# Kernel optimization log

Measured on AMD Instinct MI355X. Metric: run time of the kernel, lower is better.

## Reference

```python
import jax, jax.numpy as jnp
import numpy as np

NEG_INF = -1e30  # large negative instead of float('-inf') for fp16/bf16 safety in softmax


def setup_inputs() -> dict:
    key = jax.random.key(0)
    k1, k2, k3, k4 = jax.random.split(key, 4)
    B, T, C, H = 8, 2048, 768, 64
    x = jax.random.normal(k1, (B, T, C), dtype=jnp.float32)
    # nn.Linear(n_embd, head_size, bias=False): y = x @ W.T, W shape (head_size, n_embd)
    s = 1.0 / np.sqrt(C)
    Wk = jax.random.uniform(k2, (H, C), dtype=jnp.float32, minval=-s, maxval=s)
    Wq = jax.random.uniform(k3, (H, C), dtype=jnp.float32, minval=-s, maxval=s)
    Wv = jax.random.uniform(k4, (H, C), dtype=jnp.float32, minval=-s, maxval=s)
    return {"x": x, "Wk": Wk, "Wq": Wq, "Wv": Wv}


def reference(x, Wk, Wq, Wv):
    # x: [B,T,C]; Wk/Wq/Wv: [H,C]
    k = jnp.einsum('btc,hc->bth', x, Wk)  # [B,T,H]
    q = jnp.einsum('btc,hc->bth', x, Wq)
    v = jnp.einsum('btc,hc->bth', x, Wv)
    att = jnp.einsum('bqh,bkh->bqk', q, k)  # [B,T,T], NOTE: no 1/sqrt(H) scaling, faithful to source
    T = x.shape[1]
    causal = jnp.tril(jnp.ones((T, T), dtype=bool))
    att = jnp.where(causal, att, NEG_INF)
    att = jax.nn.softmax(att, axis=-1)
    out = jnp.einsum('bqk,bkh->bqh', att, v)  # [B,T,H]
    return out
```

## Files before the change

kernel.cpp:

```cpp
#include <hip/hip_runtime.h>
#include <hip/hip_bf16.h>
#include <stdint.h>

typedef float    f32x4  __attribute__((ext_vector_type(4)));
typedef float    f32x16 __attribute__((ext_vector_type(16)));
typedef short    s16x8  __attribute__((ext_vector_type(8)));
typedef uint32_t u32x4  __attribute__((ext_vector_type(4)));

#define NB 8
#define NT 2048
#define NC 768
#define NH 64

__device__ __forceinline__ uint32_t f2bf1(float f) {
  union { float f; uint32_t u; } v; v.f = f;
  uint32_t u = v.u;
  return (u + 0x7fffu + ((u >> 16) & 1u)) >> 16;
}
__device__ __forceinline__ uint32_t packbf2(float lo, float hi) {
  return f2bf1(lo) | (f2bf1(hi) << 16);
}

__global__ __launch_bounds__(256) void wconv_kernel(
    const float* __restrict__ Wk, const float* __restrict__ Wq,
    const float* __restrict__ Wv, short* __restrict__ Wb)
{
  int idx = blockIdx.x * 256 + threadIdx.x;
  if (idx >= 192 * 768) return;
  int n = idx / 768;
  float v;
  if (n < 64)       v = Wq[idx];
  else if (n < 128) v = Wk[idx - 64 * 768];
  else              v = Wv[idx - 128 * 768];
  Wb[idx] = (short)f2bf1(v);
}

__global__ __launch_bounds__(256) void proj_kernel(
    const float* __restrict__ x, const short* __restrict__ Wb,
    short* __restrict__ qb, short* __restrict__ kb, short* __restrict__ vTb)
{
  __shared__ char smem[8192 + 24576];
  short* ldsX   = (short*)smem;
  float* ldsAcc = (float*)(smem + 8192);
  short* ldsV   = (short*)smem;

  const int tid  = threadIdx.x;
  const int lane = tid & 63;
  const int w    = tid >> 6;
  const int kh   = w >> 1;
  const int nh   = w & 1;
  const int col  = lane & 31;
  const int half = lane >> 5;
  const int t0   = blockIdx.x * 32;

  f32x16 acc[3];
#pragma unroll
  for (int j = 0; j < 3; ++j)
#pragma unroll
    for (int e = 0; e < 16; ++e) acc[j][e] = 0.f;

  const int sg  = tid & 127;
  const int skh = tid >> 7;
  const int sr  = sg >> 2;
  const int sf  = (sg & 3) * 16;
  const float* xsrc = x + (size_t)(t0 + sr) * NC + skh * 384 + sf;
  short* ldst = ldsX + skh * 2048 + sr * 64 + sf;

  f32x4 st[4];
#pragma unroll
  for (int u = 0; u < 4; ++u) st[u] = *(const f32x4*)(xsrc + u * 4);

  const short* wbase = Wb + kh * 384 + half * 8;

  for (int s = 0; s < 6; ++s) {
    __syncthreads();
    {
      uint32_t pw[8];
#pragma unroll
      for (int u = 0; u < 4; ++u) {
        pw[2 * u]     = packbf2(st[u][0], st[u][1]);
        pw[2 * u + 1] = packbf2(st[u][2], st[u][3]);
      }
      *(u32x4*)ldst       = (u32x4){pw[0], pw[1], pw[2], pw[3]};
      *(u32x4*)(ldst + 8) = (u32x4){pw[4], pw[5], pw[6], pw[7]};
    }
    __syncthreads();
    if (s < 5) {
#pragma unroll
      for (int u = 0; u < 4; ++u) st[u] = *(const f32x4*)(xsrc + (s + 1) * 64 + u * 4);
    }
#pragma unroll
    for (int ks = 0; ks < 4; ++ks) {
      s16x8 af = *(const s16x8*)&ldsX[kh * 2048 + col * 64 + ks * 16 + half * 8];
#pragma unroll
      for (int j = 0; j < 3; ++j) {
        int n = (nh * 3 + j) * 32 + col;
        s16x8 bf = *(const s16x8*)(wbase + (size_t)n * NC + s * 64 + ks * 16);
        acc[j] = __builtin_amdgcn_mfma_f32_32x32x16_bf16(af, bf, acc[j], 0, 0, 0);
      }
    }
  }

  if (kh == 0) {
#pragma unroll
    for (int j = 0; j < 3; ++j)
#pragma unroll
      for (int r = 0; r < 16; ++r) {
        int rd = (r & 3) + 8 * (r >> 2) + 4 * half;
        ldsAcc[rd * 192 + (nh * 3 + j) * 32 + col] = acc[j][r];
      }
  }
  __syncthreads();
  const int b  = t0 >> 11;
  const int tl = t0 & (NT - 1);
  if (kh == 1) {
#pragma unroll
    for (int j = 0; j < 3; ++j) {
      int nb = (nh * 3 + j) * 32;
#pragma unroll
      for (int r = 0; r < 16; ++r) {
        int rd = (r & 3) + 8 * (r >> 2) + 4 * half;
        float sum = acc[j][r] + ldsAcc[rd * 192 + nb + col];
        if (nb < 128) {
          short* dst = (nb < 64) ? qb : kb;
          dst[(size_t)(t0 + rd) * NH + (nb & 63) + col] = (short)f2bf1(sum);
        } else {
          ldsV[(nb - 128 + col) * 32 + rd] = (short)f2bf1(sum);
        }
      }
    }
  }
  __syncthreads();
  {
    int h = tid >> 2, off = (tid & 3) * 8;
    *(s16x8*)&vTb[(size_t)(b * NH + h) * NT + tl + off] = *(const s16x8*)&ldsV[h * 32 + off];
  }
}

__global__ __launch_bounds__(256) void attn_kernel(
    const short* __restrict__ qb, const short* __restrict__ kb,
    const short* __restrict__ vTb, float* __restrict__ out)
{
  __shared__ float ldsO[4][32][65];
  __shared__ float ldsM[4][32];
  __shared__ float ldsL[4][32];

  const int tid  = threadIdx.x;
  const int lane = tid & 63;
  const int w    = tid >> 6;
  const int col  = lane & 31;
  const int half = lane >> 5;
  const int b    = blockIdx.x >> 6;
  int qt = blockIdx.x & 63;
  if (blockIdx.x & 256) qt = 63 - qt;
  const int q0 = qt * 32;
  const int nT = qt + 1;
  const int tBeg = (w * nT) >> 2;
  const int tEnd = ((w + 1) * nT) >> 2;

  s16x8 qf[4];
  {
    const short* qptr = qb + (size_t)(b * NT + q0 + col) * NH + half * 8;
#pragma unroll
    for (int ks = 0; ks < 4; ++ks) qf[ks] = *(const s16x8*)(qptr + ks * 16);
  }

  const short* kbase = kb  + (size_t)(b * NT + col) * NH + half * 8;
  const short* vbase = vTb + (size_t)(b * NH + col) * NT + half * 8;

  f32x16 oacc[2];
#pragma unroll
  for (int t = 0; t < 2; ++t)
#pragma unroll
    for (int e = 0; e < 16; ++e) oacc[t][e] = 0.f;

  float m = -1e30f, l = 0.f;

  s16x8 rk[4], rv[4];
  auto prefetch = [&](int t) {
#pragma unroll
    for (int ks = 0; ks < 4; ++ks)
      rk[ks] = *(const s16x8*)(kbase + (size_t)t * 32 * NH + ks * 16);
#pragma unroll
    for (int i = 0; i < 4; ++i)
      rv[i] = *(const s16x8*)(vbase + (size_t)(i >> 1) * 32 * NT + t * 32 + (i & 1) * 16);
  };
  if (tBeg < tEnd) prefetch(tBeg);

  for (int t = tBeg; t < tEnd; ++t) {
    s16x8 ck[4] = {rk[0], rk[1], rk[2], rk[3]};
    s16x8 cv[4] = {rv[0], rv[1], rv[2], rv[3]};
    if (t + 1 < tEnd) prefetch(t + 1);

    f32x16 s;
#pragma unroll
    for (int e = 0; e < 16; ++e) s[e] = 0.f;
#pragma unroll
    for (int ks = 0; ks < 4; ++ks)
      s = __builtin_amdgcn_mfma_f32_32x32x16_bf16(ck[ks], qf[ks], s, 0, 0, 0);

    if (t == nT - 1) {
#pragma unroll
      for (int r = 0; r < 16; ++r) {
        int rd = (r & 3) + 8 * (r >> 2) + 4 * half;
        if (rd > col) s[r] = -1e30f;
      }
    }
    float vmax = s[0];
#pragma unroll
    for (int r = 1; r < 16; ++r) vmax = fmaxf(vmax, s[r]);
    vmax = fmaxf(vmax, __shfl_xor(vmax, 32));
    float mn    = fmaxf(m, vmax);
    float alpha = __expf(m - mn);
    float p[16];
    float rs = 0.f;
#pragma unroll
    for (int r = 0; r < 16; ++r) { p[r] = __expf(s[r] - mn); rs += p[r]; }
    rs += __shfl_xor(rs, 32);
    l = l * alpha + rs;
    m = mn;
#pragma unroll
    for (int t2 = 0; t2 < 2; ++t2)
#pragma unroll
      for (int e = 0; e < 16; ++e) oacc[t2][e] *= alpha;

    uint32_t pw[8];
#pragma unroll
    for (int i = 0; i < 8; ++i) pw[i] = packbf2(p[2 * i], p[2 * i + 1]);
#pragma unroll
    for (int kc = 0; kc < 2; ++kc) {
      uint32_t s0 = half ? pw[4 * kc]     : pw[4 * kc + 2];
      uint32_t s1 = half ? pw[4 * kc + 1] : pw[4 * kc + 3];
      uint32_t r0 = __shfl_xor(s0, 32);
      uint32_t r1 = __shfl_xor(s1, 32);
      uint32_t w0 = half ? r0 : pw[4 * kc];
      uint32_t w1 = half ? r1 : pw[4 * kc + 1];
      uint32_t w2 = half ? pw[4 * kc + 2] : r0;
      uint32_t w3 = half ? pw[4 * kc + 3] : r1;
      union { u32x4 u; s16x8 v; } pf;
      pf.u = (u32x4){w0, w1, w2, w3};
#pragma unroll
      for (int ht = 0; ht < 2; ++ht)
        oacc[ht] = __builtin_amdgcn_mfma_f32_32x32x16_bf16(cv[ht * 2 + kc], pf.v, oacc[ht], 0, 0, 0);
    }
  }

  if (half == 0) { ldsM[w][col] = m; ldsL[w][col] = l; }
#pragma unroll
  for (int ht = 0; ht < 2; ++ht)
#pragma unroll
    for (int r = 0; r < 16; ++r) {
      int rd = (r & 3) + 8 * (r >> 2) + 4 * half;
      ldsO[w][col][ht * 32 + rd] = oacc[ht][r];
    }
  __syncthreads();

  const int q  = tid >> 3;
  const int h0 = (tid & 7) * 8;
  float mv[4], lv[4];
#pragma unroll
  for (int i = 0; i < 4; ++i) { mv[i] = ldsM[i][q]; lv[i] = ldsL[i][q]; }
  float M = fmaxf(fmaxf(mv[0], mv[1]), fmaxf(mv[2], mv[3]));
  float cf[4], L = 0.f;
#pragma unroll
  for (int i = 0; i < 4; ++i) { cf[i] = __expf(mv[i] - M); L += cf[i] * lv[i]; }
  float inv = 1.0f / L;
  float o[8];
#pragma unroll
  for (int j = 0; j < 8; ++j) {
    float a = 0.f;
#pragma unroll
    for (int i = 0; i < 4; ++i) a += cf[i] * ldsO[i][q][h0 + j];
    o[j] = a * inv;
  }
  float* obase = out + (size_t)(b * NT + q0 + q) * NH + h0;
  *(f32x4*)obase       = (f32x4){o[0], o[1], o[2], o[3]};
  *(f32x4*)(obase + 4) = (f32x4){o[4], o[5], o[6], o[7]};
}

extern "C" void kernel_launch(void* const* d_in, const int* in_sizes, int n_in,
                              void* d_out, int out_size, void* d_ws, size_t ws_size,
                              hipStream_t stream) {
  const float* x  = (const float*)d_in[0];
  const float* Wk = (const float*)d_in[1];
  const float* Wq = (const float*)d_in[2];
  const float* Wv = (const float*)d_in[3];
  float* out = (float*)d_out;

  char* ws = (char*)d_ws;
  short* Wb  = (short*)(ws);
  short* qb  = (short*)(ws + 524288);
  short* kb  = (short*)(ws + 524288 + 2097152);
  short* vTb = (short*)(ws + 524288 + 2 * 2097152);

  hipLaunchKernelGGL(wconv_kernel, dim3(576), dim3(256), 0, stream, Wk, Wq, Wv, Wb);
  hipLaunchKernelGGL(proj_kernel,  dim3(512), dim3(256), 0, stream, x, Wb, qb, kb, vTb);
  hipLaunchKernelGGL(attn_kernel,  dim3(512), dim3(256), 0, stream, qb, kb, vTb, out);
}
```

Baseline: 132.7 us.

## Use 8 waves per attention block with tree merge, exp2 softmax, bulk-staged projection

The attention kernel now runs 512 threads (8 waves), each handling an eighth of the key tiles. Partial softmax states are combined with a log-tree merge in LDS, and the output is staged through LDS for coalesced stores. Q is pre-scaled by log2(e) so the softmax can use exp2f. The projection kernel loads the whole 32x768 x tile into swizzled LDS in one shot instead of a 6-stage loop, and packs pairs with the HIP bf16x2 intrinsic. These aim at more latency hiding and less exp and sync cost, at the price of more LDS and register pressure and extra barriers during the merge.

```diff
diff --git a/kernel.cpp b/kernel.cpp
--- a/kernel.cpp
+++ b/kernel.cpp
@@ -11,6 +11,7 @@
 #define NT 2048
 #define NC 768
 #define NH 64
+#define LOG2E 1.4426950408889634f
 
 __device__ __forceinline__ uint32_t f2bf1(float f) {
   union { float f; uint32_t u; } v; v.f = f;
@@ -18,7 +19,9 @@
   return (u + 0x7fffu + ((u >> 16) & 1u)) >> 16;
 }
 __device__ __forceinline__ uint32_t packbf2(float lo, float hi) {
-  return f2bf1(lo) | (f2bf1(hi) << 16);
+  union { __hip_bfloat162 h; uint32_t u; } c;
+  c.h = __float22bfloat162_rn(float2{lo, hi});
+  return c.u;
 }
 
 __global__ __launch_bounds__(256) void wconv_kernel(
@@ -35,14 +38,14 @@
   Wb[idx] = (short)f2bf1(v);
 }
 
-__global__ __launch_bounds__(256) void proj_kernel(
+__global__ __launch_bounds__(256, 2) void proj_kernel(
     const float* __restrict__ x, const short* __restrict__ Wb,
     short* __restrict__ qb, short* __restrict__ kb, short* __restrict__ vTb)
 {
-  __shared__ char smem[8192 + 24576];
+  __shared__ char smem[49152 + 4096];
   short* ldsX   = (short*)smem;
-  float* ldsAcc = (float*)(smem + 8192);
-  short* ldsV   = (short*)smem;
+  float* ldsAcc = (float*)smem;
+  short* ldsV   = (short*)(smem + 49152);
 
   const int tid  = threadIdx.x;
   const int lane = tid & 63;
@@ -53,54 +56,48 @@
   const int half = lane >> 5;
   const int t0   = blockIdx.x * 32;
 
+  {
+    const int tok = tid >> 3;
+    const int g   = tid & 7;
+    const float* src = x + (size_t)(t0 + tok) * NC + g * 8;
+    f32x4 st[12][2];
+#pragma unroll
+    for (int c = 0; c < 12; ++c) {
+      st[c][0] = *(const f32x4*)(src + c * 64);
+      st[c][1] = *(const f32x4*)(src + c * 64 + 4);
+    }
+    short* dst = ldsX + tok * 64 + ((g ^ (tok & 7)) << 3);
+#pragma unroll
+    for (int c = 0; c < 12; ++c) {
+      u32x4 pw = {packbf2(st[c][0][0], st[c][0][1]), packbf2(st[c][0][2], st[c][0][3]),
+                  packbf2(st[c][1][0], st[c][1][1]), packbf2(st[c][1][2], st[c][1][3])};
+      *(u32x4*)(dst + c * 2048) = pw;
+    }
+  }
+  __syncthreads();
+
   f32x16 acc[3];
 #pragma unroll
   for (int j = 0; j < 3; ++j)
 #pragma unroll
     for (int e = 0; e < 16; ++e) acc[j][e] = 0.f;
 
-  const int sg  = tid & 127;
-  const int skh = tid >> 7;
-  const int sr  = sg >> 2;
-  const int sf  = (sg & 3) * 16;
-  const float* xsrc = x + (size_t)(t0 + sr) * NC + skh * 384 + sf;
-  short* ldst = ldsX + skh * 2048 + sr * 64 + sf;
-
-  f32x4 st[4];
-#pragma unroll
-  for (int u = 0; u < 4; ++u) st[u] = *(const f32x4*)(xsrc + u * 4);
-
-  const short* wbase = Wb + kh * 384 + half * 8;
-
-  for (int s = 0; s < 6; ++s) {
-    __syncthreads();
-    {
-      uint32_t pw[8];
-#pragma unroll
-      for (int u = 0; u < 4; ++u) {
-        pw[2 * u]     = packbf2(st[u][0], st[u][1]);
-        pw[2 * u + 1] = packbf2(st[u][2], st[u][3]);
-      }
-      *(u32x4*)ldst       = (u32x4){pw[0], pw[1], pw[2], pw[3]};
-      *(u32x4*)(ldst + 8) = (u32x4){pw[4], pw[5], pw[6], pw[7]};
-    }
-    __syncthreads();
-    if (s < 5) {
-#pragma unroll
-      for (int u = 0; u < 4; ++u) st[u] = *(const f32x4*)(xsrc + (s + 1) * 64 + u * 4);
-    }
+#pragma unroll
+  for (int c6 = 0; c6 < 6; ++c6) {
+    const int c = kh * 6 + c6;
 #pragma unroll
     for (int ks = 0; ks < 4; ++ks) {
-      s16x8 af = *(const s16x8*)&ldsX[kh * 2048 + col * 64 + ks * 16 + half * 8];
+      s16x8 af = *(const s16x8*)&ldsX[c * 2048 + col * 64 + (((ks * 2 + half) ^ (col & 7)) << 3)];
 #pragma unroll
       for (int j = 0; j < 3; ++j) {
         int n = (nh * 3 + j) * 32 + col;
-        s16x8 bf = *(const s16x8*)(wbase + (size_t)n * NC + s * 64 + ks * 16);
+        s16x8 bf = *(const s16x8*)&Wb[(size_t)n * NC + c * 64 + ks * 16 + half * 8];
         acc[j] = __builtin_amdgcn_mfma_f32_32x32x16_bf16(af, bf, acc[j], 0, 0, 0);
       }
     }
   }
 
+  __syncthreads();
   if (kh == 0) {
 #pragma unroll
     for (int j = 0; j < 3; ++j)
@@ -121,9 +118,10 @@
       for (int r = 0; r < 16; ++r) {
         int rd = (r & 3) + 8 * (r >> 2) + 4 * half;
         float sum = acc[j][r] + ldsAcc[rd * 192 + nb + col];
-        if (nb < 128) {
-          short* dst = (nb < 64) ? qb : kb;
-          dst[(size_t)(t0 + rd) * NH + (nb & 63) + col] = (short)f2bf1(sum);
+        if (nb < 64) {
+          qb[(size_t)(t0 + rd) * NH + nb + col] = (short)f2bf1(sum * LOG2E);
+        } else if (nb < 128) {
+          kb[(size_t)(t0 + rd) * NH + (nb - 64) + col] = (short)f2bf1(sum);
         } else {
           ldsV[(nb - 128 + col) * 32 + rd] = (short)f2bf1(sum);
         }
@@ -137,7 +135,7 @@
   }
 }
 
-__global__ __launch_bounds__(256) void attn_kernel(
+__global__ __launch_bounds__(512, 4) void attn_kernel(
     const short* __restrict__ qb, const short* __restrict__ kb,
     const short* __restrict__ vTb, float* __restrict__ out)
 {
@@ -155,8 +153,8 @@
   if (blockIdx.x & 256) qt = 63 - qt;
   const int q0 = qt * 32;
   const int nT = qt + 1;
-  const int tBeg = (w * nT) >> 2;
-  const int tEnd = ((w + 1) * nT) >> 2;
+  const int tBeg = (w * nT) >> 3;
+  const int tEnd = ((w + 1) * nT) >> 3;
 
   s16x8 qf[4];
   {
@@ -211,11 +209,11 @@
     for (int r = 1; r < 16; ++r) vmax = fmaxf(vmax, s[r]);
     vmax = fmaxf(vmax, __shfl_xor(vmax, 32));
     float mn    = fmaxf(m, vmax);
-    float alpha = __expf(m - mn);
+    float alpha = exp2f(m - mn);
     float p[16];
     float rs = 0.f;
 #pragma unroll
-    for (int r = 0; r < 16; ++r) { p[r] = __expf(s[r] - mn); rs += p[r]; }
+    for (int r = 0; r < 16; ++r) { p[r] = exp2f(s[r] - mn); rs += p[r]; }
     rs += __shfl_xor(rs, 32);
     l = l * alpha + rs;
     m = mn;
@@ -245,37 +243,58 @@
     }
   }
 
-  if (half == 0) { ldsM[w][col] = m; ldsL[w][col] = l; }
-#pragma unroll
-  for (int ht = 0; ht < 2; ++ht)
-#pragma unroll
-    for (int r = 0; r < 16; ++r) {
-      int rd = (r & 3) + 8 * (r >> 2) + 4 * half;
-      ldsO[w][col][ht * 32 + rd] = oacc[ht][r];
-    }
-  __syncthreads();
-
-  const int q  = tid >> 3;
-  const int h0 = (tid & 7) * 8;
-  float mv[4], lv[4];
-#pragma unroll
-  for (int i = 0; i < 4; ++i) { mv[i] = ldsM[i][q]; lv[i] = ldsL[i][q]; }
-  float M = fmaxf(fmaxf(mv[0], mv[1]), fmaxf(mv[2], mv[3]));
-  float cf[4], L = 0.f;
-#pragma unroll
-  for (int i = 0; i < 4; ++i) { cf[i] = __expf(mv[i] - M); L += cf[i] * lv[i]; }
-  float inv = 1.0f / L;
-  float o[8];
-#pragma unroll
-  for (int j = 0; j < 8; ++j) {
-    float a = 0.f;
-#pragma unroll
-    for (int i = 0; i < 4; ++i) a += cf[i] * ldsO[i][q][h0 + j];
-    o[j] = a * inv;
-  }
-  float* obase = out + (size_t)(b * NT + q0 + q) * NH + h0;
-  *(f32x4*)obase       = (f32x4){o[0], o[1], o[2], o[3]};
-  *(f32x4*)(obase + 4) = (f32x4){o[4], o[5], o[6], o[7]};
+  auto writeSlot = [&](int slot) {
+    if (half == 0) { ldsM[slot][col] = m; ldsL[slot][col] = l; }
+#pragma unroll
+    for (int ht = 0; ht < 2; ++ht)
+#pragma unroll
+      for (int r = 0; r < 16; ++r) {
+        int rd = (r & 3) + 8 * (r >> 2) + 4 * half;
+        ldsO[slot][col][ht * 32 + rd] = oacc[ht][r];
+      }
+  };
+  auto mergeFrom = [&](int slot) {
+    float mb = ldsM[slot][col];
+    float lb = ldsL[slot][col];
+    float M2 = fmaxf(m, mb);
+    float ca = exp2f(m - M2), cb = exp2f(mb - M2);
+    l = ca * l + cb * lb;
+    m = M2;
+#pragma unroll
+    for (int ht = 0; ht < 2; ++ht)
+#pragma unroll
+      for (int r = 0; r < 16; ++r) {
+        int rd = (r & 3) + 8 * (r >> 2) + 4 * half;
+        oacc[ht][r] = ca * oacc[ht][r] + cb * ldsO[slot][col][ht * 32 + rd];
+      }
+  };
+
+  if (w >= 4) writeSlot(w - 4);
+  __syncthreads();
+  if (w < 4) mergeFrom(w);
+  __syncthreads();
+  if (w == 2 || w == 3) writeSlot(w - 2);
+  __syncthreads();
+  if (w < 2) mergeFrom(w);
+  __syncthreads();
+  if (w == 1) writeSlot(0);
+  __syncthreads();
+  if (w == 0) {
+    mergeFrom(0);
+    float inv = 1.0f / l;
+#pragma unroll
+    for (int ht = 0; ht < 2; ++ht)
+#pragma unroll
+      for (int r = 0; r < 16; ++r) {
+        int rd = (r & 3) + 8 * (r >> 2) + 4 * half;
+        ldsO[0][col][ht * 32 + rd] = oacc[ht][r] * inv;
+      }
+  }
+  __syncthreads();
+  {
+    int q = tid >> 4, off = (tid & 15) * 4;
+    *(f32x4*)(out + (size_t)(b * NT + q0 + q) * NH + off) = *(const f32x4*)&ldsO[0][q][off];
+  }
 }
 
 extern "C" void kernel_launch(void* const* d_in, const int* in_sizes, int n_in,
@@ -295,5 +314,5 @@
 
   hipLaunchKernelGGL(wconv_kernel, dim3(576), dim3(256), 0, stream, Wk, Wq, Wv, Wb);
   hipLaunchKernelGGL(proj_kernel,  dim3(512), dim3(256), 0, stream, x, Wb, qb, kb, vTb);
-  hipLaunchKernelGGL(attn_kernel,  dim3(512), dim3(256), 0, stream, qb, kb, vTb, out);
-}
+  hipLaunchKernelGGL(attn_kernel,  dim3(512), dim3(512), 0, stream, qb, kb, vTb, out);
+}
```

Result: slower. 148.6 us (+12.0%).

## Store Q/K/V in MFMA fragment layout, restructure projection and double-buffer attention

Applied to the files above, without the earlier changes.

The projection kernel now runs 512 threads with a 4-way K split. It loads x directly from global memory into registers and converts it to bf16 without staging through LDS, then reduces the partial sums through LDS. Q, K and V are written in a pre-swizzled MFMA-fragment layout, with Q pre-scaled by log2(e), so attention can use exp2 and issue contiguous per-lane loads. The attention loop now double-buffers K/V tiles across two register sets, and bf16 packing uses the HIP intrinsic. Together these aim to cut LDS traffic and load latency, at the cost of higher register pressure and extra sync stages in the reduction.

```diff
diff --git a/kernel.cpp b/kernel.cpp
--- a/kernel.cpp
+++ b/kernel.cpp
@@ -11,6 +11,7 @@
 #define NT 2048
 #define NC 768
 #define NH 64
+#define LOG2E 1.4426950408889634f
 
 __device__ __forceinline__ uint32_t f2bf1(float f) {
   union { float f; uint32_t u; } v; v.f = f;
@@ -18,7 +19,9 @@
   return (u + 0x7fffu + ((u >> 16) & 1u)) >> 16;
 }
 __device__ __forceinline__ uint32_t packbf2(float lo, float hi) {
-  return f2bf1(lo) | (f2bf1(hi) << 16);
+  union { __hip_bfloat162 h; uint32_t u; } c;
+  c.h = __float22bfloat162_rn(float2{lo, hi});
+  return c.u;
 }
 
 __global__ __launch_bounds__(256) void wconv_kernel(
@@ -35,14 +38,14 @@
   Wb[idx] = (short)f2bf1(v);
 }
 
-__global__ __launch_bounds__(256) void proj_kernel(
+__global__ __launch_bounds__(512, 2) void proj_kernel(
     const float* __restrict__ x, const short* __restrict__ Wb,
-    short* __restrict__ qb, short* __restrict__ kb, short* __restrict__ vTb)
+    short* __restrict__ qf_buf, short* __restrict__ kf_buf, short* __restrict__ vf_buf)
 {
-  __shared__ char smem[8192 + 24576];
-  short* ldsX   = (short*)smem;
-  float* ldsAcc = (float*)(smem + 8192);
-  short* ldsV   = (short*)smem;
+  __shared__ float slots[4 * 3072];
+  short* ldsQT = (short*)slots;
+  short* ldsKT = (short*)slots + 2176;
+  short* ldsVT = (short*)slots + 4352;
 
   const int tid  = threadIdx.x;
   const int lane = tid & 63;
@@ -53,93 +56,113 @@
   const int half = lane >> 5;
   const int t0   = blockIdx.x * 32;
 
+  const float* xsrc = x + (size_t)(t0 + col) * NC + kh * 192 + half * 8;
+  const short* w0 = Wb + (size_t)((nh * 3 + 0) * 32 + col) * NC + kh * 192 + half * 8;
+  const short* w1 = w0 + 32 * NC;
+  const short* w2 = w1 + 32 * NC;
+
   f32x16 acc[3];
 #pragma unroll
   for (int j = 0; j < 3; ++j)
 #pragma unroll
     for (int e = 0; e < 16; ++e) acc[j][e] = 0.f;
 
-  const int sg  = tid & 127;
-  const int skh = tid >> 7;
-  const int sr  = sg >> 2;
-  const int sf  = (sg & 3) * 16;
-  const float* xsrc = x + (size_t)(t0 + sr) * NC + skh * 384 + sf;
-  short* ldst = ldsX + skh * 2048 + sr * 64 + sf;
-
-  f32x4 st[4];
-#pragma unroll
-  for (int u = 0; u < 4; ++u) st[u] = *(const f32x4*)(xsrc + u * 4);
-
-  const short* wbase = Wb + kh * 384 + half * 8;
-
-  for (int s = 0; s < 6; ++s) {
-    __syncthreads();
-    {
-      uint32_t pw[8];
-#pragma unroll
-      for (int u = 0; u < 4; ++u) {
-        pw[2 * u]     = packbf2(st[u][0], st[u][1]);
-        pw[2 * u + 1] = packbf2(st[u][2], st[u][3]);
-      }
-      *(u32x4*)ldst       = (u32x4){pw[0], pw[1], pw[2], pw[3]};
-      *(u32x4*)(ldst + 8) = (u32x4){pw[4], pw[5], pw[6], pw[7]};
-    }
-    __syncthreads();
-    if (s < 5) {
-#pragma unroll
-      for (int u = 0; u < 4; ++u) st[u] = *(const f32x4*)(xsrc + (s + 1) * 64 + u * 4);
-    }
-#pragma unroll
-    for (int ks = 0; ks < 4; ++ks) {
-      s16x8 af = *(const s16x8*)&ldsX[kh * 2048 + col * 64 + ks * 16 + half * 8];
-#pragma unroll
-      for (int j = 0; j < 3; ++j) {
-        int n = (nh * 3 + j) * 32 + col;
-        s16x8 bf = *(const s16x8*)(wbase + (size_t)n * NC + s * 64 + ks * 16);
-        acc[j] = __builtin_amdgcn_mfma_f32_32x32x16_bf16(af, bf, acc[j], 0, 0, 0);
-      }
-    }
-  }
-
+  f32x4 xA[2], xB[2];
+  s16x8 wA[3], wB[3];
+  auto loadS = [&](f32x4* xr, s16x8* wr, int ks) {
+    xr[0] = *(const f32x4*)(xsrc + ks * 16);
+    xr[1] = *(const f32x4*)(xsrc + ks * 16 + 4);
+    wr[0] = *(const s16x8*)(w0 + ks * 16);
+    wr[1] = *(const s16x8*)(w1 + ks * 16);
+    wr[2] = *(const s16x8*)(w2 + ks * 16);
+  };
+  auto computeS = [&](f32x4* xr, s16x8* wr) {
+    union { u32x4 u; s16x8 v; } af;
+    af.u = (u32x4){packbf2(xr[0][0], xr[0][1]), packbf2(xr[0][2], xr[0][3]),
+                   packbf2(xr[1][0], xr[1][1]), packbf2(xr[1][2], xr[1][3])};
+    acc[0] = __builtin_amdgcn_mfma_f32_32x32x16_bf16(af.v, wr[0], acc[0], 0, 0, 0);
+    acc[1] = __builtin_amdgcn_mfma_f32_32x32x16_bf16(af.v, wr[1], acc[1], 0, 0, 0);
+    acc[2] = __builtin_amdgcn_mfma_f32_32x32x16_bf16(af.v, wr[2], acc[2], 0, 0, 0);
+  };
+
+  loadS(xA, wA, 0);
+#pragma unroll
+  for (int ks = 0; ks < 12; ks += 2) {
+    loadS(xB, wB, ks + 1);
+    computeS(xA, wA);
+    if (ks + 2 < 12) loadS(xA, wA, ks + 2);
+    computeS(xB, wB);
+  }
+
+  if (kh >= 2) {
+    float* sl = slots + ((kh - 2) * 2 + nh) * 3072;
+#pragma unroll
+    for (int j = 0; j < 3; ++j)
+#pragma unroll
+      for (int r = 0; r < 16; ++r) {
+        int rd = (r & 3) + 8 * (r >> 2) + 4 * half;
+        sl[rd * 96 + j * 32 + col] = acc[j][r];
+      }
+  }
+  __syncthreads();
+  if (kh < 2) {
+    float* sl = slots + (kh * 2 + nh) * 3072;
+#pragma unroll
+    for (int j = 0; j < 3; ++j)
+#pragma unroll
+      for (int r = 0; r < 16; ++r) {
+        int rd = (r & 3) + 8 * (r >> 2) + 4 * half;
+        acc[j][r] += sl[rd * 96 + j * 32 + col];
+      }
+  }
+  __syncthreads();
+  if (kh == 1) {
+    float* sl = slots + (2 + nh) * 3072;
+#pragma unroll
+    for (int j = 0; j < 3; ++j)
+#pragma unroll
+      for (int r = 0; r < 16; ++r) {
+        int rd = (r & 3) + 8 * (r >> 2) + 4 * half;
+        sl[rd * 96 + j * 32 + col] = acc[j][r];
+      }
+  }
+  __syncthreads();
   if (kh == 0) {
+    float* sl = slots + (2 + nh) * 3072;
 #pragma unroll
     for (int j = 0; j < 3; ++j)
 #pragma unroll
       for (int r = 0; r < 16; ++r) {
         int rd = (r & 3) + 8 * (r >> 2) + 4 * half;
-        ldsAcc[rd * 192 + (nh * 3 + j) * 32 + col] = acc[j][r];
-      }
-  }
-  __syncthreads();
-  const int b  = t0 >> 11;
-  const int tl = t0 & (NT - 1);
-  if (kh == 1) {
-#pragma unroll
-    for (int j = 0; j < 3; ++j) {
-      int nb = (nh * 3 + j) * 32;
-#pragma unroll
-      for (int r = 0; r < 16; ++r) {
-        int rd = (r & 3) + 8 * (r >> 2) + 4 * half;
-        float sum = acc[j][r] + ldsAcc[rd * 192 + nb + col];
-        if (nb < 128) {
-          short* dst = (nb < 64) ? qb : kb;
-          dst[(size_t)(t0 + rd) * NH + (nb & 63) + col] = (short)f2bf1(sum);
-        } else {
-          ldsV[(nb - 128 + col) * 32 + rd] = (short)f2bf1(sum);
-        }
-      }
-    }
-  }
-  __syncthreads();
+        float sum = acc[j][r] + sl[rd * 96 + j * 32 + col];
+        int nn = nh * 96 + j * 32 + col;
+        if (nn < 64)        ldsQT[rd * 68 + nn]        = (short)f2bf1(sum * LOG2E);
+        else if (nn < 128)  ldsKT[rd * 68 + (nn - 64)] = (short)f2bf1(sum);
+        else                ldsVT[(nn - 128) * 34 + rd] = (short)f2bf1(sum);
+      }
+  }
+  __syncthreads();
+
   {
-    int h = tid >> 2, off = (tid & 3) * 8;
-    *(s16x8*)&vTb[(size_t)(b * NH + h) * NT + tl + off] = *(const s16x8*)&ldsV[h * 32 + off];
-  }
-}
-
-__global__ __launch_bounds__(256) void attn_kernel(
-    const short* __restrict__ qb, const short* __restrict__ kb,
-    const short* __restrict__ vTb, float* __restrict__ out)
+    const int b  = t0 >> 11;
+    const int kt = (t0 >> 5) & 63;
+    const size_t base = ((size_t)(b * 64 + kt) * 4) * 512;
+    if (w < 4) {
+      s16x8 vq = *(const s16x8*)&ldsQT[col * 68 + w * 16 + half * 8];
+      *(s16x8*)&qf_buf[base + w * 512 + lane * 8] = vq;
+      s16x8 vk = *(const s16x8*)&ldsKT[col * 68 + w * 16 + half * 8];
+      *(s16x8*)&kf_buf[base + w * 512 + lane * 8] = vk;
+    } else {
+      int i = w - 4;
+      s16x8 vv = *(const s16x8*)&ldsVT[(col + (i >> 1) * 32) * 34 + (i & 1) * 16 + half * 8];
+      *(s16x8*)&vf_buf[base + i * 512 + lane * 8] = vv;
+    }
+  }
+}
+
+__global__ __launch_bounds__(256, 2) void attn_kernel(
+    const short* __restrict__ qf_buf, const short* __restrict__ kf_buf,
+    const short* __restrict__ vf_buf, float* __restrict__ out)
 {
   __shared__ float ldsO[4][32][65];
   __shared__ float ldsM[4][32];
@@ -160,38 +183,31 @@
 
   s16x8 qf[4];
   {
-    const short* qptr = qb + (size_t)(b * NT + q0 + col) * NH + half * 8;
-#pragma unroll
-    for (int ks = 0; ks < 4; ++ks) qf[ks] = *(const s16x8*)(qptr + ks * 16);
-  }
-
-  const short* kbase = kb  + (size_t)(b * NT + col) * NH + half * 8;
-  const short* vbase = vTb + (size_t)(b * NH + col) * NT + half * 8;
+    const short* qp = qf_buf + ((size_t)(b * 64 + qt) * 4) * 512 + lane * 8;
+#pragma unroll
+    for (int ks = 0; ks < 4; ++ks) qf[ks] = *(const s16x8*)(qp + ks * 512);
+  }
+  const short* kfb = kf_buf + (size_t)b * 64 * 2048 + lane * 8;
+  const short* vfb = vf_buf + (size_t)b * 64 * 2048 + lane * 8;
 
   f32x16 oacc[2];
 #pragma unroll
-  for (int t = 0; t < 2; ++t)
-#pragma unroll
-    for (int e = 0; e < 16; ++e) oacc[t][e] = 0.f;
-
+  for (int i = 0; i < 2; ++i)
+#pragma unroll
+    for (int e = 0; e < 16; ++e) oacc[i][e] = 0.f;
   float m = -1e30f, l = 0.f;
 
-  s16x8 rk[4], rv[4];
-  auto prefetch = [&](int t) {
-#pragma unroll
-    for (int ks = 0; ks < 4; ++ks)
-      rk[ks] = *(const s16x8*)(kbase + (size_t)t * 32 * NH + ks * 16);
-#pragma unroll
-    for (int i = 0; i < 4; ++i)
-      rv[i] = *(const s16x8*)(vbase + (size_t)(i >> 1) * 32 * NT + t * 32 + (i & 1) * 16);
+  s16x8 kA[4], vA[4], kB[4], vB[4];
+  auto loadT = [&](s16x8* dk, s16x8* dv, int t) {
+    const short* kp = kfb + (size_t)t * 2048;
+    const short* vp = vfb + (size_t)t * 2048;
+#pragma unroll
+    for (int i = 0; i < 4; ++i) {
+      dk[i] = *(const s16x8*)(kp + i * 512);
+      dv[i] = *(const s16x8*)(vp + i * 512);
+    }
   };
-  if (tBeg < tEnd) prefetch(tBeg);
-
-  for (int t = tBeg; t < tEnd; ++t) {
-    s16x8 ck[4] = {rk[0], rk[1], rk[2], rk[3]};
-    s16x8 cv[4] = {rv[0], rv[1], rv[2], rv[3]};
-    if (t + 1 < tEnd) prefetch(t + 1);
-
+  auto body = [&](s16x8* ck, s16x8* cv, int t) {
     f32x16 s;
 #pragma unroll
     for (int e = 0; e < 16; ++e) s[e] = 0.f;
@@ -211,18 +227,18 @@
     for (int r = 1; r < 16; ++r) vmax = fmaxf(vmax, s[r]);
     vmax = fmaxf(vmax, __shfl_xor(vmax, 32));
     float mn    = fmaxf(m, vmax);
-    float alpha = __expf(m - mn);
+    float alpha = exp2f(m - mn);
     float p[16];
     float rs = 0.f;
 #pragma unroll
-    for (int r = 0; r < 16; ++r) { p[r] = __expf(s[r] - mn); rs += p[r]; }
+    for (int r = 0; r < 16; ++r) { p[r] = exp2f(s[r] - mn); rs += p[r]; }
     rs += __shfl_xor(rs, 32);
     l = l * alpha + rs;
     m = mn;
 #pragma unroll
-    for (int t2 = 0; t2 < 2; ++t2)
-#pragma unroll
-      for (int e = 0; e < 16; ++e) oacc[t2][e] *= alpha;
+    for (int i = 0; i < 2; ++i)
+#pragma unroll
+      for (int e = 0; e < 16; ++e) oacc[i][e] *= alpha;
 
     uint32_t pw[8];
 #pragma unroll
@@ -243,7 +259,18 @@
       for (int ht = 0; ht < 2; ++ht)
         oacc[ht] = __builtin_amdgcn_mfma_f32_32x32x16_bf16(cv[ht * 2 + kc], pf.v, oacc[ht], 0, 0, 0);
     }
-  }
+  };
+
+  int t = tBeg;
+  if (t < tEnd) loadT(kA, vA, t);
+  if (t + 1 < tEnd) loadT(kB, vB, t + 1);
+  for (; t + 1 < tEnd; t += 2) {
+    body(kA, vA, t);
+    if (t + 2 < tEnd) loadT(kA, vA, t + 2);
+    body(kB, vB, t + 1);
+    if (t + 3 < tEnd) loadT(kB, vB, t + 3);
+  }
+  if (t < tEnd) body(kA, vA, t);
 
   if (half == 0) { ldsM[w][col] = m; ldsL[w][col] = l; }
 #pragma unroll
@@ -263,7 +290,7 @@
   float M = fmaxf(fmaxf(mv[0], mv[1]), fmaxf(mv[2], mv[3]));
   float cf[4], L = 0.f;
 #pragma unroll
-  for (int i = 0; i < 4; ++i) { cf[i] = __expf(mv[i] - M); L += cf[i] * lv[i]; }
+  for (int i = 0; i < 4; ++i) { cf[i] = exp2f(mv[i] - M); L += cf[i] * lv[i]; }
   float inv = 1.0f / L;
   float o[8];
 #pragma unroll
@@ -289,11 +316,11 @@
 
   char* ws = (char*)d_ws;
   short* Wb  = (short*)(ws);
-  short* qb  = (short*)(ws + 524288);
-  short* kb  = (short*)(ws + 524288 + 2097152);
-  short* vTb = (short*)(ws + 524288 + 2 * 2097152);
+  short* qfb = (short*)(ws + (512 << 10));
+  short* kfb = (short*)(ws + (512 << 10) + (2 << 20));
+  short* vfb = (short*)(ws + (512 << 10) + (4 << 20));
 
   hipLaunchKernelGGL(wconv_kernel, dim3(576), dim3(256), 0, stream, Wk, Wq, Wv, Wb);
-  hipLaunchKernelGGL(proj_kernel,  dim3(512), dim3(256), 0, stream, x, Wb, qb, kb, vTb);
-  hipLaunchKernelGGL(attn_kernel,  dim3(512), dim3(256), 0, stream, qb, kb, vTb, out);
-}
+  hipLaunchKernelGGL(proj_kernel,  dim3(512), dim3(512), 0, stream, x, Wb, qfb, kfb, vfb);
+  hipLaunchKernelGGL(attn_kernel,  dim3(512), dim3(256), 0, stream, qfb, kfb, vfb, out);
+}
```

After: 133.4 us. No clear change (+0.6%).
